# Kernel tuning notes

Hardware: AMD Instinct MI355X
Metric: run time of the kernel (lower is better)

The kernel has to match this reference:

```python
import jax, jax.numpy as jnp
import numpy as np

B, M, D = 16384, 40, 32
INPUT_DIM = M * D  # 1280
CIN_SIZES = [128, 128]
DEEP_DIMS = [256, 128, 64]
EPS = 1e-5


def _init_linear(key, fan_in, fan_out):
    k1, k2 = jax.random.split(key)
    bound = 1.0 / np.sqrt(fan_in)
    w = jax.random.uniform(k1, (fan_out, fan_in), jnp.float32, -bound, bound)
    b = jax.random.uniform(k2, (fan_out,), jnp.float32, -bound, bound)
    return w, b


def setup_inputs() -> dict:
    key = jax.random.key(0)
    ks = jax.random.split(key, 12)
    x = jax.random.normal(ks[0], (B, INPUT_DIM), jnp.float32)
    emb_3d = jax.random.normal(ks[1], (B, M, D), jnp.float32)
    lin_w, lin_b = _init_linear(ks[2], INPUT_DIM, 1)
    # CIN conv1d (kernel_size=1) weights, flattened to [out, in]
    conv_w0, conv_b0 = _init_linear(ks[3], M * M, CIN_SIZES[0])          # in = 40*40
    prev1 = CIN_SIZES[0] // 2                                             # split_half
    conv_w1, conv_b1 = _init_linear(ks[4], M * prev1, CIN_SIZES[1])       # in = 40*64
    cin_out_dim = CIN_SIZES[0] // 2 + CIN_SIZES[1]                        # 192
    cin_out_w, cin_out_b = _init_linear(ks[5], cin_out_dim, 1)
    dims = [INPUT_DIM] + DEEP_DIMS
    deep_w0, deep_b0 = _init_linear(ks[6], dims[0], dims[1])
    deep_w1, deep_b1 = _init_linear(ks[7], dims[1], dims[2])
    deep_w2, deep_b2 = _init_linear(ks[8], dims[2], dims[3])
    ln_g0, ln_b0 = jnp.ones((dims[1],), jnp.float32), jnp.zeros((dims[1],), jnp.float32)
    ln_g1, ln_b1 = jnp.ones((dims[2],), jnp.float32), jnp.zeros((dims[2],), jnp.float32)
    ln_g2, ln_b2 = jnp.ones((dims[3],), jnp.float32), jnp.zeros((dims[3],), jnp.float32)
    return dict(x=x, emb_3d=emb_3d, lin_w=lin_w, lin_b=lin_b,
                conv_w0=conv_w0, conv_b0=conv_b0, conv_w1=conv_w1, conv_b1=conv_b1,
                cin_out_w=cin_out_w, cin_out_b=cin_out_b,
                deep_w0=deep_w0, deep_b0=deep_b0, ln_g0=ln_g0, ln_b0=ln_b0,
                deep_w1=deep_w1, deep_b1=deep_b1, ln_g1=ln_g1, ln_b1=ln_b1,
                deep_w2=deep_w2, deep_b2=deep_b2, ln_g2=ln_g2, ln_b2=ln_b2)


def _layernorm(h, g, b):
    mu = jnp.mean(h, axis=-1, keepdims=True)
    var = jnp.mean(jnp.square(h - mu), axis=-1, keepdims=True)
    return (h - mu) * jax.lax.rsqrt(var + EPS) * g + b


def _cin_layer(x0, xi, w, b):
    # outer = einsum('bmd,bnd->bmnd') then 1x1 conv over flattened (m*n).
    # Fused: contract the (m,n) outer product directly with the conv weight.
    o = w.shape[0]
    m, n = x0.shape[1], xi.shape[1]
    w3 = w.reshape(o, m, n)
    out = jnp.einsum('bmd,bnd,omn->bod', x0, xi, w3) + b[None, :, None]
    return jax.nn.relu(out)


def reference(x, emb_3d, lin_w, lin_b,
              conv_w0, conv_b0, conv_w1, conv_b1, cin_out_w, cin_out_b,
              deep_w0, deep_b0, ln_g0, ln_b0,
              deep_w1, deep_b1, ln_g1, ln_b1,
              deep_w2, deep_b2, ln_g2, ln_b2):
    aux = (x @ lin_w.T + lin_b)[:, 0]  # [B]

    # CIN with split_half=True
    x0 = emb_3d                                   # [B, 40, 32]
    out0 = _cin_layer(x0, x0, conv_w0, conv_b0)    # [B, 128, 32]
    h1, direct0 = jnp.split(out0, 2, axis=1)       # hidden gets FIRST half
    out1 = _cin_layer(x0, h1, conv_w1, conv_b1)    # [B, 128, 32]
    cin_feat = jnp.sum(jnp.concatenate([direct0, out1], axis=1), axis=2)  # [B, 192]
    aux = aux + (cin_feat @ cin_out_w.T + cin_out_b)[:, 0]

    # Deep tower (dropout = identity in eval)
    h = jax.nn.relu(_layernorm(x @ deep_w0.T + deep_b0, ln_g0, ln_b0))
    h = jax.nn.relu(_layernorm(h @ deep_w1.T + deep_b1, ln_g1, ln_b1))
    h = jax.nn.relu(_layernorm(h @ deep_w2.T + deep_b2, ln_g2, ln_b2))
    return h, aux
```

## Files before the change

kernel.cpp:

```cpp
#include <hip/hip_runtime.h>
#include <hip/hip_bf16.h>

typedef unsigned int u32;
typedef __attribute__((ext_vector_type(8))) short short8;
typedef __attribute__((ext_vector_type(8))) _Float16 half8;
typedef __attribute__((ext_vector_type(4))) float f32x4;

__device__ __forceinline__ u32 bf16_rne(float f) {
  u32 u = __builtin_bit_cast(u32, f);
  return (u + 0x7fffu + ((u >> 16) & 1u)) >> 16;
}
__device__ __forceinline__ u32 pk_bf16(float a, float b) {
  union { __hip_bfloat162 h; u32 u; } cv;
  cv.h = __float22bfloat162_rn(make_float2(a, b));
  return cv.u;
}
__device__ __forceinline__ unsigned short f16b(float f) {
  return __builtin_bit_cast(unsigned short, (_Float16)f);
}
__device__ __forceinline__ half8 splat8(_Float16 x) {
  return (half8){x, x, x, x, x, x, x, x};
}

__device__ __forceinline__ void glds16(const u32* g, u32* l) {
  __builtin_amdgcn_global_load_lds((const __attribute__((address_space(1))) u32*)g,
                                   (__attribute__((address_space(3))) u32*)l, 16, 0, 0);
}

__global__ void swz_kernel(const float* __restrict__ W, unsigned short* __restrict__ out,
                           int N, int K) {
  int tid = blockIdx.x * 256 + threadIdx.x;
  if (tid >= N * K) return;
  int j = tid & 7, l = (tid >> 3) & 63, rest = tid >> 9;
  int nt = N >> 4;
  int t = rest % nt, k32 = rest / nt;
  int o = t * 16 + (l & 15);
  int k = k32 * 32 + (l >> 4) * 8 + j;
  out[tid] = (unsigned short)bf16_rne(W[(size_t)o * K + k]);
}
__global__ void swz_f16_kernel(const float* __restrict__ W, unsigned short* __restrict__ out,
                               int N, int K) {
  int tid = blockIdx.x * 256 + threadIdx.x;
  if (tid >= N * K) return;
  int j = tid & 7, l = (tid >> 3) & 63, rest = tid >> 9;
  int nt = N >> 4;
  int t = rest % nt, k32 = rest / nt;
  int o = t * 16 + (l & 15);
  int k = k32 * 32 + (l >> 4) * 8 + j;
  out[tid] = f16b(W[(size_t)o * K + k]);
}

__global__ void tbl_kernel(u32* __restrict__ tbl0) {
  int g = threadIdx.x;
  if (g >= 120) return;
  int base = 0, m = 0;
  for (m = 0; m < 40; ++m) {
    int cnt = 5 - (m >> 3);
    if (g < base + cnt) break;
    base += cnt;
  }
  int n0 = 8 * ((m >> 3) + (g - base));
  tbl0[g] = (u32)m | ((u32)n0 << 8);
}

__global__ void swz0s_kernel(const float* __restrict__ W, const u32* __restrict__ tbl0,
                             unsigned short* __restrict__ out) {
  int tid = blockIdx.x * 256 + threadIdx.x;
  if (tid >= 960 * 128) return;
  int j = tid & 7, l = (tid >> 3) & 63, rest = tid >> 9;
  int t = rest & 7, k32 = rest >> 3;
  int o = t * 16 + (l & 15);
  int g = k32 * 4 + (l >> 4);
  u32 te = tbl0[g];
  int m = (int)(te & 255u), n0 = (int)(te >> 8);
  int n = n0 + j;
  float val;
  if (n < m) val = 0.f;
  else if (n == m) val = W[o * 1600 + m * 41];
  else val = W[o * 1600 + m * 40 + n] + W[o * 1600 + n * 40 + m];
  out[tid] = f16b(val);
}

__global__ __launch_bounds__(256, 2) void cin_kernel(
    const float* __restrict__ emb, const unsigned short* __restrict__ wz0s,
    const unsigned short* __restrict__ wz1, const u32* __restrict__ tbl0,
    const float* __restrict__ b0v, const float* __restrict__ b1v,
    const float* __restrict__ cw, float* __restrict__ aux) {
  __shared__ __align__(16) unsigned short Xh[128 * 40];
  __shared__ __align__(16) unsigned short h1s[128 * 72];
  __shared__ u32 tbl[120];
  __shared__ float auxacc[128];

  const int tid = threadIdx.x;
  const int lane = tid & 63;
  const int w = tid >> 6;
  const int wr = w >> 1, wc = w & 1;
  const int rl = lane & 15, q = lane >> 4;
  const int b0blk = blockIdx.x * 4;

#pragma unroll
  for (int i = 0; i < 5; ++i) {
    int idx = i * 256 + tid;
    int b = idx / 320;
    int rem = idx - b * 320;
    int m = rem >> 3, d0 = (rem & 7) * 4;
    float4 v = *(const float4*)(emb + ((size_t)(b0blk + b) * 40 + m) * 32 + d0);
    unsigned short* xc = &Xh[(b * 32 + d0) * 40 + m];
    xc[0] = f16b(v.x); xc[40] = f16b(v.y); xc[80] = f16b(v.z); xc[120] = f16b(v.w);
  }
  if (tid < 128) auxacc[tid] = 0.f;
  if (tid < 120) tbl[tid] = tbl0[tid];
  __syncthreads();

  f32x4 acc[4][4];
#pragma unroll
  for (int u = 0; u < 4; ++u)
#pragma unroll
    for (int t = 0; t < 4; ++t) acc[u][t] = f32x4{0.f, 0.f, 0.f, 0.f};

  {
    const u32* bptr = (const u32*)wz0s + wc * 1024 + lane * 4;
    const u32* xw = (const u32*)Xh;
    uint4 bA[4], bB[4];
    uint4 vnA[4], vnB[4];
    _Float16 xmA[4], xmB[4];

    auto loadB0 = [&](int kc, uint4* b) {
#pragma unroll
      for (int tt = 0; tt < 4; ++tt) b[tt] = *(const uint4*)(bptr + kc * 2048 + tt * 256);
    };
    auto loadA0 = [&](int kc, uint4* vn, _Float16* xm) {
      u32 te = tbl[kc * 4 + q];
      int mm = (int)(te & 255u);
      int w0 = (int)(te >> 8) >> 1;
#pragma unroll
      for (int u = 0; u < 4; ++u) {
        int r = 64 * wr + 16 * u + rl;
        vn[u] = *(const uint4*)(xw + r * 20 + w0);
        xm[u] = __builtin_bit_cast(_Float16, Xh[r * 40 + mm]);
      }
    };
    auto mfma0 = [&](const uint4* vn, const _Float16* xm, const uint4* bv) {
      __builtin_amdgcn_s_setprio(1);
#pragma unroll
      for (int u = 0; u < 4; ++u) {
        half8 af = __builtin_bit_cast(half8, vn[u]) * splat8(xm[u]);
#pragma unroll
        for (int tt = 0; tt < 4; ++tt)
          acc[u][tt] = __builtin_amdgcn_mfma_f32_16x16x32_f16(
              af, __builtin_bit_cast(half8, bv[tt]), acc[u][tt], 0, 0, 0);
      }
      __builtin_amdgcn_s_setprio(0);
    };

    loadB0(0, bA);
    loadA0(0, vnA, xmA);
    for (int kc = 0; kc < 30; kc += 2) {
      loadB0(kc + 1, bB);
      loadA0(kc + 1, vnB, xmB);
      mfma0(vnA, xmA, bA);
      int kn = (kc + 2 < 30) ? kc + 2 : 0;
      loadB0(kn, bA);
      loadA0(kn, vnA, xmA);
      mfma0(vnB, xmB, bB);
    }
  }

  if (wc == 0) {
#pragma unroll
    for (int u = 0; u < 4; ++u) {
      int r0q = 64 * wr + 16 * u + 4 * q;
#pragma unroll
      for (int tt = 0; tt < 4; ++tt) {
        int o = 16 * tt + rl;
        float bb = b0v[o];
#pragma unroll
        for (int i = 0; i < 4; ++i) {
          float vv = fmaxf(acc[u][tt][i] + bb, 0.f);
          h1s[(r0q + i) * 72 + o] = f16b(vv);
        }
      }
    }
  } else {
#pragma unroll
    for (int u = 0; u < 4; ++u)
#pragma unroll
      for (int i = 0; i < 4; ++i) {
        float sle = 0.f;
#pragma unroll
        for (int tt = 0; tt < 4; ++tt) {
          int o = 64 + 16 * tt + rl;
          sle += fmaxf(acc[u][tt][i] + b0v[o], 0.f) * cw[o - 64];
        }
        sle += __shfl_xor(sle, 1, 16);
        sle += __shfl_xor(sle, 2, 16);
        sle += __shfl_xor(sle, 4, 16);
        sle += __shfl_xor(sle, 8, 16);
        if (rl == 0) atomicAdd(&auxacc[64 * wr + 16 * u + 4 * q + i], sle);
      }
  }
#pragma unroll
  for (int u = 0; u < 4; ++u)
#pragma unroll
    for (int t = 0; t < 4; ++t) acc[u][t] = f32x4{0.f, 0.f, 0.f, 0.f};
  __syncthreads();

  {
    const u32* bptr = (const u32*)wz1 + wc * 1024 + lane * 4;
    const u32* hw = (const u32*)h1s;
    uint4 bA[4], bB[4];
    uint4 hpA[4], hpB[4];
    _Float16 xmA[4], xmB[4];

    auto loadB1 = [&](int kc, uint4* b) {
#pragma unroll
      for (int tt = 0; tt < 4; ++tt) b[tt] = *(const uint4*)(bptr + kc * 2048 + tt * 256);
    };
    auto loadH = [&](int kc, uint4* hp) {
      int wof = ((kc & 1) << 4) + 4 * q;
#pragma unroll
      for (int u = 0; u < 4; ++u) {
        int r = 64 * wr + 16 * u + rl;
        hp[u] = *(const uint4*)(hw + r * 36 + wof);
      }
    };
    auto loadXM = [&](int kp, _Float16* xm) {
#pragma unroll
      for (int u = 0; u < 4; ++u)
        xm[u] = __builtin_bit_cast(_Float16, Xh[(64 * wr + 16 * u + rl) * 40 + kp]);
    };
    auto mfma1 = [&](const uint4* hp, const _Float16* xm, const uint4* bv) {
      __builtin_amdgcn_s_setprio(1);
#pragma unroll
      for (int u = 0; u < 4; ++u) {
        half8 af = __builtin_bit_cast(half8, hp[u]) * splat8(xm[u]);
#pragma unroll
        for (int tt = 0; tt < 4; ++tt)
          acc[u][tt] = __builtin_amdgcn_mfma_f32_16x16x32_f16(
              af, __builtin_bit_cast(half8, bv[tt]), acc[u][tt], 0, 0, 0);
      }
      __builtin_amdgcn_s_setprio(0);
    };

    loadB1(0, bA);
    loadH(0, hpA);
    loadXM(0, xmA);
    for (int kp = 0; kp < 40; ++kp) {
      int kc = 2 * kp;
      loadB1(kc + 1, bB);
      loadH(kc + 1, hpB);
      mfma1(hpA, xmA, bA);
      int kc2 = (kc + 2 < 80) ? kc + 2 : 0;
      int kn = (kp + 1 < 40) ? kp + 1 : 0;
      loadB1(kc2, bA);
      loadH(kc2, hpA);
      loadXM(kn, xmB);
      mfma1(hpB, xmA, bB);
#pragma unroll
      for (int u = 0; u < 4; ++u) xmA[u] = xmB[u];
    }
  }

#pragma unroll
  for (int u = 0; u < 4; ++u)
#pragma unroll
    for (int i = 0; i < 4; ++i) {
      float sle = 0.f;
#pragma unroll
      for (int tt = 0; tt < 4; ++tt) {
        int o = 64 * wc + 16 * tt + rl;
        sle += fmaxf(acc[u][tt][i] + b1v[o], 0.f) * cw[64 + o];
      }
      sle += __shfl_xor(sle, 1, 16);
      sle += __shfl_xor(sle, 2, 16);
      sle += __shfl_xor(sle, 4, 16);
      sle += __shfl_xor(sle, 8, 16);
      if (rl == 0) atomicAdd(&auxacc[64 * wr + 16 * u + 4 * q + i], sle);
    }
  __syncthreads();
  if (tid < 4) {
    float ssum = 0.f;
    for (int d = 0; d < 32; ++d) ssum += auxacc[tid * 32 + d];
    aux[b0blk + tid] = ssum;
  }
}

template <int NT, bool AF32, bool LIN>
__global__ __launch_bounds__(256, 2) void gemm_deep64(
    const void* __restrict__ Ain, const unsigned short* __restrict__ Bswz,
    const float* __restrict__ bias, float* __restrict__ Cout, int M, int N, int K,
    const float* __restrict__ lw, const float* __restrict__ lb,
    const float* __restrict__ cb, float* __restrict__ aux) {
  __shared__ unsigned short At[64 * 40];
  __shared__ u32 Bt[NT * 256];
  const int tid = threadIdx.x, lane = tid & 63, w = tid >> 6;
  const int wc = w, rl = lane & 15, q = lane >> 4;
  const int r0 = blockIdx.x * 64, c0 = blockIdx.y * (NT * 16);
  const int ntg = N >> 4;
  constexpr int WT = NT / 4;
  f32x4 acc[4][WT];
#pragma unroll
  for (int u = 0; u < 4; ++u)
#pragma unroll
    for (int t = 0; t < WT; ++t) acc[u][t] = f32x4{0.f, 0.f, 0.f, 0.f};
  float lacc = 0.f;

  for (int kk = 0; kk < K; kk += 32) {
    __syncthreads();
    {
      int r = tid >> 2, kh = (tid & 3) * 8;
      if constexpr (AF32) {
        const float* A = (const float*)Ain;
        const float* src = A + (size_t)(r0 + r) * K + kk + kh;
        float4 v0 = *(const float4*)src;
        float4 v1 = *(const float4*)(src + 4);
        if constexpr (LIN) {
          if (blockIdx.y == 0) {
            const float* lwp = lw + kk + kh;
            lacc += v0.x * lwp[0] + v0.y * lwp[1] + v0.z * lwp[2] + v0.w * lwp[3] +
                    v1.x * lwp[4] + v1.y * lwp[5] + v1.z * lwp[6] + v1.w * lwp[7];
          }
        }
        uint4 p0;
        p0.x = pk_bf16(v0.x, v0.y); p0.y = pk_bf16(v0.z, v0.w);
        p0.z = pk_bf16(v1.x, v1.y); p0.w = pk_bf16(v1.z, v1.w);
        *(uint4*)&At[r * 40 + kh] = p0;
      } else {
        const unsigned short* A = (const unsigned short*)Ain;
        *(uint4*)&At[r * 40 + kh] = *(const uint4*)(A + (size_t)(r0 + r) * K + kk + kh);
      }
      const u32* gb = (const u32*)Bswz + ((size_t)(kk >> 5) * ntg + (c0 >> 4)) * 256;
      constexpr int WW = NT * 64;
#pragma unroll
      for (int j = 0; j < NT / 4; ++j)
        glds16(gb + w * WW + j * 256 + lane * 4, &Bt[w * WW + j * 256]);
    }
    __syncthreads();
    short8 af[4];
#pragma unroll
    for (int u = 0; u < 4; ++u) {
      uint4 av = *(const uint4*)&At[(16 * u + rl) * 40 + q * 8];
      af[u] = __builtin_bit_cast(short8, av);
    }
#pragma unroll
    for (int tt = 0; tt < WT; ++tt) {
      int tg = WT * wc + tt;
      uint4 bv = *(const uint4*)&Bt[(tg * 64 + lane) * 4];
      short8 bfv = __builtin_bit_cast(short8, bv);
#pragma unroll
      for (int u = 0; u < 4; ++u)
        acc[u][tt] = __builtin_amdgcn_mfma_f32_16x16x32_bf16(af[u], bfv, acc[u][tt], 0, 0, 0);
    }
  }
  if constexpr (LIN) {
    if (blockIdx.y == 0) {
      lacc += __shfl_xor(lacc, 1, 64);
      lacc += __shfl_xor(lacc, 2, 64);
      if ((tid & 3) == 0) aux[r0 + (tid >> 2)] += lacc + lb[0] + cb[0];
    }
  }
#pragma unroll
  for (int u = 0; u < 4; ++u) {
    int rr = r0 + 16 * u + 4 * q;
#pragma unroll
    for (int tt = 0; tt < WT; ++tt) {
      int o = c0 + (WT * wc + tt) * 16 + rl;
      float bb = bias[o];
#pragma unroll
      for (int i = 0; i < 4; ++i)
        Cout[(size_t)(rr + i) * N + o] = acc[u][tt][i] + bb;
    }
  }
}

template <int D, bool OUTF32>
__global__ void ln_relu_kernel(const float* __restrict__ in, const float* __restrict__ g,
                               const float* __restrict__ bt, void* __restrict__ out) {
  int row = blockIdx.x * 4 + (threadIdx.x >> 6);
  int lane = threadIdx.x & 63;
  constexpr int E = D / 64;
  const float* src = in + (size_t)row * D;
  float v[E], s1 = 0.f, s2 = 0.f;
#pragma unroll
  for (int e = 0; e < E; ++e) {
    v[e] = src[e * 64 + lane];
    s1 += v[e];
    s2 += v[e] * v[e];
  }
#pragma unroll
  for (int m = 1; m < 64; m <<= 1) {
    s1 += __shfl_xor(s1, m, 64);
    s2 += __shfl_xor(s2, m, 64);
  }
  float mu = s1 / (float)D;
  float rs = rsqrtf(s2 / (float)D - mu * mu + 1e-5f);
#pragma unroll
  for (int e = 0; e < E; ++e) {
    int c = e * 64 + lane;
    float y = fmaxf((v[e] - mu) * rs * g[c] + bt[c], 0.f);
    if constexpr (OUTF32)
      ((float*)out)[(size_t)row * D + c] = y;
    else
      ((unsigned short*)out)[(size_t)row * D + c] = (unsigned short)bf16_rne(y);
  }
}

extern "C" void kernel_launch(void* const* d_in, const int* in_sizes, int n_in,
                              void* d_out, int out_size, void* d_ws, size_t ws_size,
                              hipStream_t stream) {
  const float* x = (const float*)d_in[0];
  const float* emb = (const float*)d_in[1];
  const float* lin_w = (const float*)d_in[2];
  const float* lin_b = (const float*)d_in[3];
  const float* cw0 = (const float*)d_in[4];
  const float* cb0 = (const float*)d_in[5];
  const float* cw1 = (const float*)d_in[6];
  const float* cb1 = (const float*)d_in[7];
  const float* cow = (const float*)d_in[8];
  const float* cob = (const float*)d_in[9];
  const float* dw0 = (const float*)d_in[10];
  const float* db0 = (const float*)d_in[11];
  const float* g0 = (const float*)d_in[12];
  const float* be0 = (const float*)d_in[13];
  const float* dw1 = (const float*)d_in[14];
  const float* db1 = (const float*)d_in[15];
  const float* g1 = (const float*)d_in[16];
  const float* be1 = (const float*)d_in[17];
  const float* dw2 = (const float*)d_in[18];
  const float* db2 = (const float*)d_in[19];
  const float* g2 = (const float*)d_in[20];
  const float* be2 = (const float*)d_in[21];

  char* ws = (char*)d_ws;
  unsigned short* wz0s = (unsigned short*)(ws + 0);
  u32* tbl0 = (u32*)(ws + 245760);
  unsigned short* wz1 = (unsigned short*)(ws + 246272);
  unsigned short* wzd0 = (unsigned short*)(ws + 901632);
  unsigned short* wzd1 = (unsigned short*)(ws + 1556992);
  unsigned short* wzd2 = (unsigned short*)(ws + 1622528);
  float* t0 = (float*)(ws + 1638912);
  unsigned short* h0b = (unsigned short*)(ws + 18416128);
  float* t1 = (float*)(ws + 26804736);
  unsigned short* h1b = (unsigned short*)(ws + 35193344);
  float* t2 = (float*)(ws + 39387648);

  float* h_out = (float*)d_out;
  float* aux = h_out + (size_t)16384 * 64;

  tbl_kernel<<<1, 128, 0, stream>>>(tbl0);
  swz0s_kernel<<<480, 256, 0, stream>>>(cw0, tbl0, wz0s);
  swz_f16_kernel<<<(2560 * 128 + 255) / 256, 256, 0, stream>>>(cw1, wz1, 128, 2560);
  swz_kernel<<<(1280 * 256 + 255) / 256, 256, 0, stream>>>(dw0, wzd0, 256, 1280);
  swz_kernel<<<(256 * 128 + 255) / 256, 256, 0, stream>>>(dw1, wzd1, 128, 256);
  swz_kernel<<<(128 * 64 + 255) / 256, 256, 0, stream>>>(dw2, wzd2, 64, 128);

  cin_kernel<<<4096, 256, 0, stream>>>(emb, wz0s, wz1, tbl0, cb0, cb1, cow, aux);

  gemm_deep64<8, true, true><<<dim3(256, 2), 256, 0, stream>>>(
      x, wzd0, db0, t0, 16384, 256, 1280, lin_w, lin_b, cob, aux);
  ln_relu_kernel<256, false><<<4096, 256, 0, stream>>>(t0, g0, be0, h0b);
  gemm_deep64<8, false, false><<<dim3(256, 1), 256, 0, stream>>>(
      h0b, wzd1, db1, t1, 16384, 128, 256, nullptr, nullptr, nullptr, nullptr);
  ln_relu_kernel<128, false><<<4096, 256, 0, stream>>>(t1, g1, be1, h1b);
  gemm_deep64<4, false, false><<<dim3(256, 1), 256, 0, stream>>>(
      h1b, wzd2, db2, t2, 16384, 64, 128, nullptr, nullptr, nullptr, nullptr);
  ln_relu_kernel<64, true><<<4096, 256, 0, stream>>>(t2, g2, be2, h_out);
}
```

Before: 611.2 us.

## Fuse deep tower GEMMs and LayerNorms into one kernel with shared-memory intermediates

Replaces three GEMM launches and three LayerNorm launches with a single tower kernel. Each block handles 32 rows, keeps the hidden activations in shared memory as bf16, and applies bias, LayerNorm and ReLU in the MFMA epilogue. This removes the global round trips of the fp32 intermediates (about 17MB plus smaller tensors) and several launches. The cost is 512 blocks of 32 rows each, which gives less weight reuse per block in the 1280-wide first GEMM, and a non-pipelined K loop.

```diff
diff --git a/kernel.cpp b/kernel.cpp
--- a/kernel.cpp
+++ b/kernel.cpp
@@ -285,124 +285,178 @@
   }
 }
 
-template <int NT, bool AF32, bool LIN>
-__global__ __launch_bounds__(256, 2) void gemm_deep64(
-    const void* __restrict__ Ain, const unsigned short* __restrict__ Bswz,
-    const float* __restrict__ bias, float* __restrict__ Cout, int M, int N, int K,
+template <int NT, bool LAST>
+__device__ __forceinline__ void ln_epilogue(
+    int tid, int w, int rl, int q, f32x4 (&acc)[2][4],
+    const float* __restrict__ bias, const float* __restrict__ g,
+    const float* __restrict__ be, float* rs1, float* rs2,
+    unsigned short* hout, int hstr, float* __restrict__ Cout, int r0) {
+  constexpr int WT = NT / 4;
+  constexpr float rN = 1.0f / (float)(NT * 16);
+  __syncthreads();
+  if (tid < 32) { rs1[tid] = 0.f; rs2[tid] = 0.f; }
+  __syncthreads();
+  float vals[2][WT][4];
+#pragma unroll
+  for (int u = 0; u < 2; ++u)
+#pragma unroll
+    for (int tt = 0; tt < WT; ++tt) {
+      int o = (WT * w + tt) * 16 + rl;
+      float bb = bias[o];
+#pragma unroll
+      for (int i = 0; i < 4; ++i) vals[u][tt][i] = acc[u][tt][i] + bb;
+    }
+#pragma unroll
+  for (int u = 0; u < 2; ++u)
+#pragma unroll
+    for (int i = 0; i < 4; ++i) {
+      float s1 = 0.f, s2 = 0.f;
+#pragma unroll
+      for (int tt = 0; tt < WT; ++tt) {
+        float v = vals[u][tt][i];
+        s1 += v;
+        s2 += v * v;
+      }
+#pragma unroll
+      for (int m = 1; m < 16; m <<= 1) {
+        s1 += __shfl_xor(s1, m, 64);
+        s2 += __shfl_xor(s2, m, 64);
+      }
+      if (rl == 0) {
+        atomicAdd(&rs1[16 * u + 4 * q + i], s1);
+        atomicAdd(&rs2[16 * u + 4 * q + i], s2);
+      }
+    }
+  __syncthreads();
+#pragma unroll
+  for (int u = 0; u < 2; ++u)
+#pragma unroll
+    for (int i = 0; i < 4; ++i) {
+      int row = 16 * u + 4 * q + i;
+      float mu = rs1[row] * rN;
+      float rsd = rsqrtf(rs2[row] * rN - mu * mu + 1e-5f);
+#pragma unroll
+      for (int tt = 0; tt < WT; ++tt) {
+        int o = (WT * w + tt) * 16 + rl;
+        float y = fmaxf((vals[u][tt][i] - mu) * rsd * g[o] + be[o], 0.f);
+        if constexpr (LAST)
+          Cout[(size_t)(r0 + row) * (NT * 16) + o] = y;
+        else
+          hout[row * hstr + o] = (unsigned short)bf16_rne(y);
+      }
+    }
+}
+
+__global__ __launch_bounds__(256, 2) void tower_kernel(
+    const float* __restrict__ x, const unsigned short* __restrict__ wzd0,
+    const unsigned short* __restrict__ wzd1, const unsigned short* __restrict__ wzd2,
+    const float* __restrict__ db0, const float* __restrict__ g0, const float* __restrict__ be0,
+    const float* __restrict__ db1, const float* __restrict__ g1, const float* __restrict__ be1,
+    const float* __restrict__ db2, const float* __restrict__ g2, const float* __restrict__ be2,
     const float* __restrict__ lw, const float* __restrict__ lb,
-    const float* __restrict__ cb, float* __restrict__ aux) {
-  __shared__ unsigned short At[64 * 40];
-  __shared__ u32 Bt[NT * 256];
+    const float* __restrict__ cb, float* __restrict__ aux, float* __restrict__ hout) {
+  __shared__ __align__(16) u32 Bt[4096];
+  __shared__ __align__(16) unsigned short At[32 * 40];
+  __shared__ __align__(16) unsigned short h0[32 * 264];
+  __shared__ __align__(16) unsigned short h1[32 * 136];
+  __shared__ float rs1[32], rs2[32];
+
   const int tid = threadIdx.x, lane = tid & 63, w = tid >> 6;
-  const int wc = w, rl = lane & 15, q = lane >> 4;
-  const int r0 = blockIdx.x * 64, c0 = blockIdx.y * (NT * 16);
-  const int ntg = N >> 4;
-  constexpr int WT = NT / 4;
-  f32x4 acc[4][WT];
-#pragma unroll
-  for (int u = 0; u < 4; ++u)
-#pragma unroll
-    for (int t = 0; t < WT; ++t) acc[u][t] = f32x4{0.f, 0.f, 0.f, 0.f};
+  const int rl = lane & 15, q = lane >> 4;
+  const int r0 = blockIdx.x * 32;
+
+  f32x4 acc[2][4];
+#pragma unroll
+  for (int u = 0; u < 2; ++u)
+#pragma unroll
+    for (int t = 0; t < 4; ++t) acc[u][t] = f32x4{0.f, 0.f, 0.f, 0.f};
   float lacc = 0.f;
 
-  for (int kk = 0; kk < K; kk += 32) {
+  for (int kk = 0; kk < 1280; kk += 32) {
     __syncthreads();
     {
-      int r = tid >> 2, kh = (tid & 3) * 8;
-      if constexpr (AF32) {
-        const float* A = (const float*)Ain;
-        const float* src = A + (size_t)(r0 + r) * K + kk + kh;
-        float4 v0 = *(const float4*)src;
-        float4 v1 = *(const float4*)(src + 4);
-        if constexpr (LIN) {
-          if (blockIdx.y == 0) {
-            const float* lwp = lw + kk + kh;
-            lacc += v0.x * lwp[0] + v0.y * lwp[1] + v0.z * lwp[2] + v0.w * lwp[3] +
-                    v1.x * lwp[4] + v1.y * lwp[5] + v1.z * lwp[6] + v1.w * lwp[7];
-          }
-        }
-        uint4 p0;
-        p0.x = pk_bf16(v0.x, v0.y); p0.y = pk_bf16(v0.z, v0.w);
-        p0.z = pk_bf16(v1.x, v1.y); p0.w = pk_bf16(v1.z, v1.w);
-        *(uint4*)&At[r * 40 + kh] = p0;
-      } else {
-        const unsigned short* A = (const unsigned short*)Ain;
-        *(uint4*)&At[r * 40 + kh] = *(const uint4*)(A + (size_t)(r0 + r) * K + kk + kh);
-      }
-      const u32* gb = (const u32*)Bswz + ((size_t)(kk >> 5) * ntg + (c0 >> 4)) * 256;
-      constexpr int WW = NT * 64;
-#pragma unroll
-      for (int j = 0; j < NT / 4; ++j)
-        glds16(gb + w * WW + j * 256 + lane * 4, &Bt[w * WW + j * 256]);
+      int r = tid >> 3, kh = (tid & 7) * 4;
+      const float* src = x + (size_t)(r0 + r) * 1280 + kk + kh;
+      float4 v0 = *(const float4*)src;
+      const float* lwp = lw + kk + kh;
+      lacc += v0.x * lwp[0] + v0.y * lwp[1] + v0.z * lwp[2] + v0.w * lwp[3];
+      uint2 p;
+      p.x = pk_bf16(v0.x, v0.y);
+      p.y = pk_bf16(v0.z, v0.w);
+      *(uint2*)&At[r * 40 + kh] = p;
+      const u32* gb = (const u32*)wzd0 + (size_t)(kk >> 5) * 4096;
+#pragma unroll
+      for (int j = 0; j < 4; ++j)
+        glds16(gb + w * 1024 + j * 256 + lane * 4, &Bt[w * 1024 + j * 256]);
     }
     __syncthreads();
-    short8 af[4];
-#pragma unroll
-    for (int u = 0; u < 4; ++u) {
-      uint4 av = *(const uint4*)&At[(16 * u + rl) * 40 + q * 8];
-      af[u] = __builtin_bit_cast(short8, av);
-    }
-#pragma unroll
-    for (int tt = 0; tt < WT; ++tt) {
-      int tg = WT * wc + tt;
-      uint4 bv = *(const uint4*)&Bt[(tg * 64 + lane) * 4];
-      short8 bfv = __builtin_bit_cast(short8, bv);
-#pragma unroll
-      for (int u = 0; u < 4; ++u)
+    short8 af[2];
+#pragma unroll
+    for (int u = 0; u < 2; ++u)
+      af[u] = __builtin_bit_cast(short8, *(const uint4*)&At[(16 * u + rl) * 40 + q * 8]);
+#pragma unroll
+    for (int tt = 0; tt < 4; ++tt) {
+      short8 bfv = __builtin_bit_cast(short8, *(const uint4*)&Bt[((4 * w + tt) * 64 + lane) * 4]);
+#pragma unroll
+      for (int u = 0; u < 2; ++u)
         acc[u][tt] = __builtin_amdgcn_mfma_f32_16x16x32_bf16(af[u], bfv, acc[u][tt], 0, 0, 0);
     }
   }
-  if constexpr (LIN) {
-    if (blockIdx.y == 0) {
-      lacc += __shfl_xor(lacc, 1, 64);
-      lacc += __shfl_xor(lacc, 2, 64);
-      if ((tid & 3) == 0) aux[r0 + (tid >> 2)] += lacc + lb[0] + cb[0];
-    }
-  }
-#pragma unroll
-  for (int u = 0; u < 4; ++u) {
-    int rr = r0 + 16 * u + 4 * q;
-#pragma unroll
-    for (int tt = 0; tt < WT; ++tt) {
-      int o = c0 + (WT * wc + tt) * 16 + rl;
-      float bb = bias[o];
-#pragma unroll
-      for (int i = 0; i < 4; ++i)
-        Cout[(size_t)(rr + i) * N + o] = acc[u][tt][i] + bb;
-    }
-  }
-}
-
-template <int D, bool OUTF32>
-__global__ void ln_relu_kernel(const float* __restrict__ in, const float* __restrict__ g,
-                               const float* __restrict__ bt, void* __restrict__ out) {
-  int row = blockIdx.x * 4 + (threadIdx.x >> 6);
-  int lane = threadIdx.x & 63;
-  constexpr int E = D / 64;
-  const float* src = in + (size_t)row * D;
-  float v[E], s1 = 0.f, s2 = 0.f;
-#pragma unroll
-  for (int e = 0; e < E; ++e) {
-    v[e] = src[e * 64 + lane];
-    s1 += v[e];
-    s2 += v[e] * v[e];
-  }
-#pragma unroll
-  for (int m = 1; m < 64; m <<= 1) {
-    s1 += __shfl_xor(s1, m, 64);
-    s2 += __shfl_xor(s2, m, 64);
-  }
-  float mu = s1 / (float)D;
-  float rs = rsqrtf(s2 / (float)D - mu * mu + 1e-5f);
-#pragma unroll
-  for (int e = 0; e < E; ++e) {
-    int c = e * 64 + lane;
-    float y = fmaxf((v[e] - mu) * rs * g[c] + bt[c], 0.f);
-    if constexpr (OUTF32)
-      ((float*)out)[(size_t)row * D + c] = y;
-    else
-      ((unsigned short*)out)[(size_t)row * D + c] = (unsigned short)bf16_rne(y);
-  }
+  lacc += __shfl_xor(lacc, 1, 64);
+  lacc += __shfl_xor(lacc, 2, 64);
+  lacc += __shfl_xor(lacc, 4, 64);
+  if ((tid & 7) == 0) aux[r0 + (tid >> 3)] += lacc + lb[0] + cb[0];
+
+  ln_epilogue<16, false>(tid, w, rl, q, acc, db0, g0, be0, rs1, rs2, h0, 264, nullptr, r0);
+
+#pragma unroll
+  for (int u = 0; u < 2; ++u)
+#pragma unroll
+    for (int t = 0; t < 4; ++t) acc[u][t] = f32x4{0.f, 0.f, 0.f, 0.f};
+  for (int kk = 0; kk < 256; kk += 32) {
+    __syncthreads();
+    {
+      const u32* gb = (const u32*)wzd1 + (size_t)(kk >> 5) * 2048;
+#pragma unroll
+      for (int j = 0; j < 2; ++j)
+        glds16(gb + w * 512 + j * 256 + lane * 4, &Bt[w * 512 + j * 256]);
+    }
+    __syncthreads();
+    short8 af[2];
+#pragma unroll
+    for (int u = 0; u < 2; ++u)
+      af[u] = __builtin_bit_cast(short8, *(const uint4*)&h0[(16 * u + rl) * 264 + kk + q * 8]);
+#pragma unroll
+    for (int tt = 0; tt < 2; ++tt) {
+      short8 bfv = __builtin_bit_cast(short8, *(const uint4*)&Bt[((2 * w + tt) * 64 + lane) * 4]);
+#pragma unroll
+      for (int u = 0; u < 2; ++u)
+        acc[u][tt] = __builtin_amdgcn_mfma_f32_16x16x32_bf16(af[u], bfv, acc[u][tt], 0, 0, 0);
+    }
+  }
+  ln_epilogue<8, false>(tid, w, rl, q, acc, db1, g1, be1, rs1, rs2, h1, 136, nullptr, r0);
+
+#pragma unroll
+  for (int u = 0; u < 2; ++u)
+#pragma unroll
+    for (int t = 0; t < 4; ++t) acc[u][t] = f32x4{0.f, 0.f, 0.f, 0.f};
+  for (int kk = 0; kk < 128; kk += 32) {
+    __syncthreads();
+    {
+      const u32* gb = (const u32*)wzd2 + (size_t)(kk >> 5) * 1024;
+      glds16(gb + w * 256 + lane * 4, &Bt[w * 256]);
+    }
+    __syncthreads();
+    short8 af[2];
+#pragma unroll
+    for (int u = 0; u < 2; ++u)
+      af[u] = __builtin_bit_cast(short8, *(const uint4*)&h1[(16 * u + rl) * 136 + kk + q * 8]);
+    short8 bfv = __builtin_bit_cast(short8, *(const uint4*)&Bt[(w * 64 + lane) * 4]);
+#pragma unroll
+    for (int u = 0; u < 2; ++u)
+      acc[u][0] = __builtin_amdgcn_mfma_f32_16x16x32_bf16(af[u], bfv, acc[u][0], 0, 0, 0);
+  }
+  ln_epilogue<4, true>(tid, w, rl, q, acc, db2, g2, be2, rs1, rs2, nullptr, 0, hout, r0);
 }
 
 extern "C" void kernel_launch(void* const* d_in, const int* in_sizes, int n_in,
@@ -438,11 +492,6 @@
   unsigned short* wzd0 = (unsigned short*)(ws + 901632);
   unsigned short* wzd1 = (unsigned short*)(ws + 1556992);
   unsigned short* wzd2 = (unsigned short*)(ws + 1622528);
-  float* t0 = (float*)(ws + 1638912);
-  unsigned short* h0b = (unsigned short*)(ws + 18416128);
-  float* t1 = (float*)(ws + 26804736);
-  unsigned short* h1b = (unsigned short*)(ws + 35193344);
-  float* t2 = (float*)(ws + 39387648);
 
   float* h_out = (float*)d_out;
   float* aux = h_out + (size_t)16384 * 64;
@@ -456,13 +505,6 @@
 
   cin_kernel<<<4096, 256, 0, stream>>>(emb, wz0s, wz1, tbl0, cb0, cb1, cow, aux);
 
-  gemm_deep64<8, true, true><<<dim3(256, 2), 256, 0, stream>>>(
-      x, wzd0, db0, t0, 16384, 256, 1280, lin_w, lin_b, cob, aux);
-  ln_relu_kernel<256, false><<<4096, 256, 0, stream>>>(t0, g0, be0, h0b);
-  gemm_deep64<8, false, false><<<dim3(256, 1), 256, 0, stream>>>(
-      h0b, wzd1, db1, t1, 16384, 128, 256, nullptr, nullptr, nullptr, nullptr);
-  ln_relu_kernel<128, false><<<4096, 256, 0, stream>>>(t1, g1, be1, h1b);
-  gemm_deep64<4, false, false><<<dim3(256, 1), 256, 0, stream>>>(
-      h1b, wzd2, db2, t2, 16384, 64, 128, nullptr, nullptr, nullptr, nullptr);
-  ln_relu_kernel<64, true><<<4096, 256, 0, stream>>>(t2, g2, be2, h_out);
-}
+  tower_kernel<<<512, 256, 0, stream>>>(x, wzd0, wzd1, wzd2, db0, g0, be0, db1, g1, be1,
+                                        db2, g2, be2, lin_w, lin_b, cob, aux, h_out);
+}
```

After: 606.2 us. Within noise of the previous version (-0.8%).
